# Optimization experiments

Measured on AMD Instinct MI355X. Metric: run time of the kernel, lower is better.

Reference implementation:

```python
import jax, jax.numpy as jnp
import numpy as np

N_FEAT = 128      # node_feat_size
HID = 128         # hidden_size
NUM_SEM = 64
N_ITER = 2
E_TYPES = 8
MAX_CHILDS = 65536
NUM_EDGES = 1048576


def setup_inputs() -> dict:
    key = jax.random.key(0)
    ks = jax.random.split(key, 12)
    d_in = N_FEAT + NUM_SEM
    inp = {
        "child_feats": jax.random.normal(ks[0], (1, MAX_CHILDS, d_in), jnp.float32),
        "child_exists": jax.random.uniform(ks[1], (1, MAX_CHILDS, 1), jnp.float32),
        "edge_type_onehot": jax.random.uniform(ks[2], (1, NUM_EDGES, E_TYPES), jnp.float32),
        "edge_indices": jax.random.randint(ks[3], (1, NUM_EDGES, 2), 0, MAX_CHILDS, jnp.int32),
        # learned params (PyTorch Linear: y = x @ W.T + b; store transposed)
        "W_child": jax.random.normal(ks[4], (d_in, HID), jnp.float32) / np.sqrt(d_in),
        "b_child": jnp.zeros((HID,), jnp.float32),
        "W_edge": jax.random.normal(ks[5], (N_ITER, 2 * HID + E_TYPES, HID), jnp.float32) / np.sqrt(2 * HID + E_TYPES),
        "b_edge": jnp.zeros((N_ITER, HID), jnp.float32),
        "W_parent": jax.random.normal(ks[6], ((N_ITER + 1) * HID, N_FEAT), jnp.float32) / np.sqrt((N_ITER + 1) * HID),
        "b_parent": jnp.zeros((N_FEAT,), jnp.float32),
    }
    return inp


def reference(child_feats, child_exists, edge_type_onehot, edge_indices,
              W_child, b_child, W_edge, b_edge, W_parent, b_parent):
    # batch_size == 1 enforced by original module
    x = jax.nn.relu(child_feats[0] @ W_child + b_child) * child_exists[0]  # (N, H)
    src = edge_indices[0, :, 0]  # (E,)
    dst = edge_indices[0, :, 1]  # (E,)
    ef = edge_type_onehot[0]     # (E, T)

    # node_symmetric_type == 'max' readout
    parent_feats = [jnp.max(x, axis=0)]
    for i in range(N_ITER):
        # gather endpoints, concat with edge features, small MLP
        nef = jnp.concatenate([x[src], x[dst], ef], axis=1)          # (E, 2H+T)
        nef = jax.nn.relu(nef @ W_edge[i] + b_edge[i])               # (E, H)
        # edge_symmetric_type == 'sum' -> scatter_add to source nodes
        x = jax.ops.segment_sum(nef, src, num_segments=MAX_CHILDS)   # (N, H)
        parent_feats.append(jnp.max(x, axis=0))

    parent_feat = jnp.concatenate(parent_feats)[None, :]             # (1, (I+1)*H)
    return jax.nn.relu(parent_feat @ W_parent + b_parent)            # (1, node_feat)
```

## Files before the change

kernel.cpp:

```cpp
#include <hip/hip_runtime.h>
#include <hip/hip_bf16.h>

#define HID 128
#define DIN 192
#define NCH 65536
#define NE  1048576

typedef __bf16 bfrag __attribute__((ext_vector_type(8)));
typedef float  ffrag __attribute__((ext_vector_type(4)));
typedef long   lfrag2 __attribute__((ext_vector_type(2)));

static __device__ __forceinline__ __bf16 f2bf(float x) { return (__bf16)x; }
static __device__ __forceinline__ unsigned pk2(float a, float b) {
    __bf16 b0 = f2bf(a), b1 = f2bf(b);
    return (unsigned)*(unsigned short*)&b0 | ((unsigned)*(unsigned short*)&b1 << 16);
}
static __device__ __forceinline__ unsigned char f2q(float x) {
    return (unsigned char)(__builtin_amdgcn_cvt_pk_fp8_f32(x, x, 0, false) & 0xff);
}

struct FragsQ { long d[4]; long ef; };

static __device__ __forceinline__ void stage_wfrag(
    __bf16* Wl, const float* W, int rowoff, int chunks, int t)
{
    for (int c = t; c < chunks; c += 256) {
        int lane = c & 63, u = (c >> 6) & 7, kt = c >> 9;
        int k0 = kt * 32 + ((lane >> 4) << 3), h = u * 16 + (lane & 15);
        const float* src = W + (size_t)(rowoff + k0) * 128 + h;
        bfrag f;
        #pragma unroll
        for (int j = 0; j < 8; ++j) f[j] = f2bf(src[(size_t)j * 128]);
        *(bfrag*)(&Wl[(size_t)c << 3]) = f;
    }
}

__global__ __launch_bounds__(256) void k_childhist(
    const float* __restrict__ cf, const float* __restrict__ exists,
    const float* __restrict__ Wc, const float* __restrict__ bc,
    __bf16* __restrict__ xA, unsigned int* __restrict__ pmax,
    const int* __restrict__ eidx, int* __restrict__ deg)
{
    if (blockIdx.x >= 1024) {
        const int base = (blockIdx.x - 1024) * 1024 + threadIdx.x;
        #pragma unroll
        for (int k = 0; k < 4; ++k)
            atomicAdd(&deg[eidx[2 * (base + k * 256)]], 1);
        return;
    }

    __shared__ __bf16 Wl[6 * 8 * 64 * 8];
    __shared__ float  bl[HID];
    __shared__ unsigned int cm[HID];
    const int t = threadIdx.x;

    stage_wfrag(Wl, Wc, 0, 3072, t);
    for (int idx = t; idx < HID; idx += 256) { bl[idx] = bc[idx]; cm[idx] = 0u; }
    __syncthreads();

    const int wave = t >> 6, lane = t & 63;
    const int m = lane & 15, quad = lane >> 4;

    const int tile = blockIdx.x * 4 + wave;
    const int r0 = tile << 4;
    const int row = r0 + m;

    ffrag acc[8];
    #pragma unroll
    for (int u = 0; u < 8; ++u)
        #pragma unroll
        for (int r = 0; r < 4; ++r) acc[u][r] = 0.f;

    const float* arow = cf + (size_t)row * DIN + quad * 8;
    #pragma unroll
    for (int kt = 0; kt < 6; ++kt) {
        float4 f0 = *(const float4*)(arow + kt * 32);
        float4 f1 = *(const float4*)(arow + kt * 32 + 4);
        bfrag a;
        a[0]=f2bf(f0.x); a[1]=f2bf(f0.y); a[2]=f2bf(f0.z); a[3]=f2bf(f0.w);
        a[4]=f2bf(f1.x); a[5]=f2bf(f1.y); a[6]=f2bf(f1.z); a[7]=f2bf(f1.w);
        #pragma unroll
        for (int u = 0; u < 8; ++u) {
            bfrag b = *(const bfrag*)(&Wl[(((kt * 8 + u) * 64 + lane) << 3)]);
            acc[u] = __builtin_amdgcn_mfma_f32_16x16x32_bf16(a, b, acc[u], 0, 0, 0);
        }
    }

    float mxu[8];
    #pragma unroll
    for (int u = 0; u < 8; ++u) mxu[u] = 0.f;

    #pragma unroll
    for (int r = 0; r < 4; ++r) {
        int er = r0 + quad * 4 + r;
        float exv = exists[er];
        __bf16* orow = xA + (size_t)er * HID;
        #pragma unroll
        for (int u = 0; u < 8; ++u) {
            int col = u * 16 + m;
            float v = fmaxf(acc[u][r] + bl[col], 0.f) * exv;
            orow[col] = f2bf(v);
            mxu[u] = fmaxf(mxu[u], v);
        }
    }
    #pragma unroll
    for (int u = 0; u < 8; ++u) {
        float v = mxu[u];
        v = fmaxf(v, __shfl_xor(v, 16));
        v = fmaxf(v, __shfl_xor(v, 32));
        if (quad == 0) atomicMax(&cm[u * 16 + m], __float_as_uint(v));
    }
    __syncthreads();
    if (t < HID) atomicMax(&pmax[t], cm[t]);
}

__global__ __launch_bounds__(256) void k_scan1(
    const int* __restrict__ deg, int* __restrict__ bsum)
{
    const int b = blockIdx.x, t = threadIdx.x;
    int v = deg[b * 256 + t];
    #pragma unroll
    for (int o = 1; o < 64; o <<= 1) v += __shfl_xor(v, o);
    __shared__ int ws[4];
    if ((t & 63) == 0) ws[t >> 6] = v;
    __syncthreads();
    if (t == 0) bsum[b] = ws[0] + ws[1] + ws[2] + ws[3];
}

__global__ __launch_bounds__(256) void k_scan23(
    const int* __restrict__ deg, const int* __restrict__ bsum,
    int* __restrict__ off, int* __restrict__ cursor)
{
    __shared__ int sb[256], sc[256];
    const int b = blockIdx.x, t = threadIdx.x;
    int w = bsum[t];
    int v = deg[b * 256 + t];
    sb[t] = w; sc[t] = v;
    __syncthreads();
    for (int o = 1; o < 256; o <<= 1) {
        int u1 = (t >= o) ? sb[t - o] : 0;
        int u2 = (t >= o) ? sc[t - o] : 0;
        __syncthreads();
        sb[t] += u1; sc[t] += u2;
        __syncthreads();
    }
    int bbase = (b == 0) ? 0 : sb[b - 1];
    int excl = bbase + sc[t] - v;
    off[b * 256 + t] = excl;
    cursor[b * 256 + t] = excl;
    if (b == 255 && t == 255) off[NCH] = excl + v;
}

__global__ __launch_bounds__(256) void k_scsrc(
    const __bf16* __restrict__ xCur, const float* __restrict__ We,
    const float* __restrict__ be, __bf16* __restrict__ St2,
    unsigned char* __restrict__ Dq,
    const int* __restrict__ eidx, int* __restrict__ cursor,
    const float* __restrict__ ef,
    int* __restrict__ dsts, unsigned char* __restrict__ efs8)
{
    __shared__ __bf16 Wl[4 * 8 * 64 * 8];
    __shared__ float  bl[HID];
    const int t = threadIdx.x;

    if (blockIdx.x >= 1024) {
        int e = (blockIdx.x - 1024) * 256 + t;
        int s = eidx[2 * e], d = eidx[2 * e + 1];
        const float4* p = (const float4*)(ef + (size_t)e * 8);
        float4 f0 = p[0], f1 = p[1];
        int pos = atomicAdd(&cursor[s], 1);
        dsts[pos] = d;
        unsigned p01 = __builtin_amdgcn_cvt_pk_fp8_f32(f0.x, f0.y, 0, false) & 0xffff;
        unsigned p23 = __builtin_amdgcn_cvt_pk_fp8_f32(f0.z, f0.w, 0, false) & 0xffff;
        unsigned p45 = __builtin_amdgcn_cvt_pk_fp8_f32(f1.x, f1.y, 0, false) & 0xffff;
        unsigned p67 = __builtin_amdgcn_cvt_pk_fp8_f32(f1.z, f1.w, 0, false) & 0xffff;
        unsigned long long v = (unsigned long long)(p01 | (p23 << 16))
                             | ((unsigned long long)(p45 | (p67 << 16)) << 32);
        *(unsigned long long*)(efs8 + (size_t)pos * 8) = v;
        return;
    }

    const int wave = t >> 6, lane = t & 63;
    const int m = lane & 15, quad = lane >> 4;
    const int tile = blockIdx.x * 4 + wave;
    const int r0 = tile << 4;
    const int row = r0 + m;

    stage_wfrag(Wl, We, 0, 2048, t);
    for (int idx = t; idx < HID; idx += 256) bl[idx] = be[idx];
    __syncthreads();

    bfrag a[4];
    const __bf16* ar = xCur + (size_t)row * HID + quad * 8;
    #pragma unroll
    for (int kt = 0; kt < 4; ++kt) a[kt] = *(const bfrag*)(ar + kt * 32);

    ffrag acc[8];
    #pragma unroll
    for (int u = 0; u < 8; ++u)
        #pragma unroll
        for (int r = 0; r < 4; ++r) acc[u][r] = 0.f;

    #pragma unroll
    for (int kt = 0; kt < 4; ++kt)
        #pragma unroll
        for (int u = 0; u < 8; ++u) {
            bfrag b = *(const bfrag*)(&Wl[(((kt * 8 + u) * 64 + lane) << 3)]);
            acc[u] = __builtin_amdgcn_mfma_f32_16x16x32_bf16(a[kt], b, acc[u], 0, 0, 0);
        }
    #pragma unroll
    for (int r = 0; r < 4; ++r) {
        int node = r0 + quad * 4 + r;
        bfrag pk;
        #pragma unroll
        for (int u = 0; u < 8; ++u) pk[u] = f2bf(acc[u][r] + bl[u * 16 + m]);
        *(bfrag*)(St2 + ((size_t)node * 16 + m) * 8) = pk;
    }
    __syncthreads();

    stage_wfrag(Wl, We, 128, 2048, t);
    __syncthreads();

    #pragma unroll
    for (int u = 0; u < 8; ++u)
        #pragma unroll
        for (int r = 0; r < 4; ++r) acc[u][r] = 0.f;

    #pragma unroll
    for (int kt = 0; kt < 4; ++kt)
        #pragma unroll
        for (int u = 0; u < 8; ++u) {
            bfrag b = *(const bfrag*)(&Wl[(((kt * 8 + u) * 64 + lane) << 3)]);
            acc[u] = __builtin_amdgcn_mfma_f32_16x16x32_bf16(a[kt], b, acc[u], 0, 0, 0);
        }
    #pragma unroll
    for (int r = 0; r < 4; ++r) {
        int node = r0 + quad * 4 + r;
        unsigned char* orow = Dq + (size_t)node * 128;
        #pragma unroll
        for (int u = 0; u < 8; ++u)
            orow[((u & 1) * 2 + (m >> 3)) * 32 + (u >> 1) * 8 + (m & 7)] = f2q(acc[u][r]);
    }
}

__global__ __launch_bounds__(256) void k_edge2(
    const unsigned char* __restrict__ Dq,
    const int*    __restrict__ offs,
    const int*    __restrict__ dsts,
    const unsigned char* __restrict__ efs8,
    const __bf16* __restrict__ St2,
    const float*  __restrict__ We,
    __bf16* __restrict__ xNext,
    unsigned int* __restrict__ pmax, int stage)
{
    __shared__ unsigned char Wf[8 * 16 * 8];
    __shared__ unsigned int cm[HID];
    const int t = threadIdx.x;

    if (t < HID) cm[t] = 0u;
    for (int idx = t; idx < 8 * HID; idx += 256) {
        int k2 = idx >> 7, h = idx & 127;
        Wf[((((h >> 4) * 16) + (h & 15)) << 3) + k2] = f2q(We[(size_t)(256 + k2) * HID + h]);
    }
    __syncthreads();

    const int wave = t >> 6, lane = t & 63;
    const int m = lane & 15, quad = lane >> 4;
    const int gw = blockIdx.x * 4 + wave;
    const int n0 = gw * 4;

    const long BevQ = (quad == (m >> 3))     ? ((long)0x38 << (8 * (m & 7))) : 0L;
    const long BodQ = (quad == 2 + (m >> 3)) ? ((long)0x38 << (8 * (m & 7))) : 0L;

    const int o0 = offs[n0],     o1 = offs[n0 + 1], o2 = offs[n0 + 2];
    const int o3 = offs[n0 + 3], o4 = offs[n0 + 4];

    auto selo = [&](int q) -> int {
        return (q <= 0) ? o0 : (q == 1) ? o1 : (q == 2) ? o2 : (q == 3) ? o3 : o4;
    };

    float mxu[8];
    #pragma unroll
    for (int u = 0; u < 8; ++u) mxu[u] = 0.f;

    if (o0 < o4) {
        const int dvA = dsts[min(o0 + lane, o4 - 1)];
        const int dvB = dsts[min(o0 + 64 + lane, o4 - 1)];

        auto LOADT = [&](int j) -> FragsQ {
            FragsQ f;
            int jl = j + m; jl = (jl < o4) ? jl : (o4 - 1);
            int rel = jl - o0;
            int dA = __shfl(dvA, rel & 63);
            int dB = __shfl(dvB, rel & 63);
            int dm;
            if (rel < 64)       dm = dA;
            else if (rel < 128) dm = dB;
            else                dm = dsts[jl];
            const unsigned char* rd = Dq + (size_t)dm * 128 + quad * 32;
            lfrag2 w0 = *(const lfrag2*)(rd);
            lfrag2 w1 = *(const lfrag2*)(rd + 16);
            f.d[0] = w0[0]; f.d[1] = w0[1]; f.d[2] = w1[0]; f.d[3] = w1[1];
            f.ef = (quad == 0) ? *(const long*)(efs8 + (size_t)jl * 8) : 0L;
            return f;
        };

        int ci = 0;
        while (selo(ci) == selo(ci + 1)) ++ci;
        int cj = selo(ci);

        bfrag sb = *(const bfrag*)(St2 + ((size_t)(n0 + ci) * 16 + m) * 8);
        float part[8];
        #pragma unroll
        for (int u = 0; u < 8; ++u) part[u] = 0.f;

        FragsQ aC = LOADT(cj);

        for (;;) {
            const int cEnd = selo(ci + 1);
            int ni = ci, nj = cj + 16;
            if (nj >= cEnd) {
                ni = ci + 1;
                while (ni < 4 && selo(ni) == selo(ni + 1)) ++ni;
                nj = (ni < 4) ? selo(ni) : 0;
            }
            const bool hn = (ni < 4);
            FragsQ aN;
            if (hn) aN = LOADT(nj);

            ffrag acc[8];
            #pragma unroll
            for (int u = 0; u < 8; ++u) {
                float s = (float)sb[u];
                acc[u][0] = s; acc[u][1] = s; acc[u][2] = s; acc[u][3] = s;
            }
            #pragma unroll
            for (int u = 0; u < 8; ++u)
                acc[u] = __builtin_amdgcn_mfma_f32_16x16x32_fp8_fp8(
                    aC.d[u >> 1], (u & 1) ? BodQ : BevQ, acc[u], 0, 0, 0);
            #pragma unroll
            for (int u = 0; u < 8; ++u) {
                long b = *(const long*)(&Wf[((u << 4) + m) << 3]);
                acc[u] = __builtin_amdgcn_mfma_f32_16x16x32_fp8_fp8(aC.ef, b, acc[u], 0, 0, 0);
            }

            const int rb = cj + quad * 4;
            #pragma unroll
            for (int r = 0; r < 4; ++r) {
                if (rb + r < cEnd) {
                    #pragma unroll
                    for (int u = 0; u < 8; ++u)
                        part[u] += fmaxf(acc[u][r], 0.f);
                }
            }

            if (!hn || ni != ci) {
                float tot[8];
                #pragma unroll
                for (int u = 0; u < 8; ++u) {
                    float v = part[u];
                    v += __shfl_xor(v, 16);
                    v += __shfl_xor(v, 32);
                    tot[u] = v;
                    mxu[u] = fmaxf(mxu[u], v);
                }
                float sA = (quad == 0) ? tot[0] : (quad == 1) ? tot[2] : (quad == 2) ? tot[4] : tot[6];
                float sB = (quad == 0) ? tot[1] : (quad == 1) ? tot[3] : (quad == 2) ? tot[5] : tot[7];
                const int n = n0 + ci, u0 = quad * 2;
                xNext[(size_t)n * HID + u0 * 16 + m]      = f2bf(sA);
                xNext[(size_t)n * HID + u0 * 16 + 16 + m] = f2bf(sB);
                if (hn) {
                    sb = *(const bfrag*)(St2 + ((size_t)(n0 + ni) * 16 + m) * 8);
                    #pragma unroll
                    for (int u = 0; u < 8; ++u) part[u] = 0.f;
                }
            }
            if (!hn) break;
            aC = aN; ci = ni; cj = nj;
        }
    }

    {
        const int u0 = quad * 2;
        const __bf16 zz = (__bf16)0.f;
        if (o0 == o1) { xNext[(size_t)(n0+0)*HID + u0*16 + m] = zz; xNext[(size_t)(n0+0)*HID + u0*16 + 16 + m] = zz; }
        if (o1 == o2) { xNext[(size_t)(n0+1)*HID + u0*16 + m] = zz; xNext[(size_t)(n0+1)*HID + u0*16 + 16 + m] = zz; }
        if (o2 == o3) { xNext[(size_t)(n0+2)*HID + u0*16 + m] = zz; xNext[(size_t)(n0+2)*HID + u0*16 + 16 + m] = zz; }
        if (o3 == o4) { xNext[(size_t)(n0+3)*HID + u0*16 + m] = zz; xNext[(size_t)(n0+3)*HID + u0*16 + 16 + m] = zz; }
    }

    #pragma unroll
    for (int u = 0; u < 8; ++u) {
        float v = mxu[u];
        v = fmaxf(v, __shfl_xor(v, 16));
        v = fmaxf(v, __shfl_xor(v, 32));
        if (quad == 0) atomicMax(&cm[u * 16 + m], __float_as_uint(v));
    }
    __syncthreads();
    if (t < HID) atomicMax(&pmax[stage * HID + t], cm[t]);
}

__global__ __launch_bounds__(256) void k_edge_at(
    const __bf16* __restrict__ xA, const int* __restrict__ eidx,
    const float* __restrict__ ef, const float* __restrict__ We,
    const float* __restrict__ be, float* __restrict__ xNew)
{
    __shared__ __bf16 Wl[9 * 8 * 64 * 8];
    __shared__ float  bl[HID];
    const int t = threadIdx.x;
    for (int idx = t; idx < 8 * 64 * 8; idx += 256) Wl[8 * 8 * 64 * 8 + idx] = (__bf16)0.f;
    __syncthreads();
    stage_wfrag(Wl, We, 0, 4096, t);
    for (int idx = t; idx < 8 * HID; idx += 256) {
        int k2 = idx >> 7, h = idx & 127;
        Wl[((((8 * 8) + (h >> 4)) * 64 + (h & 15)) << 3) | k2] = f2bf(We[(256 + k2) * HID + h]);
    }
    for (int idx = t; idx < HID; idx += 256) bl[idx] = be[idx];
    __syncthreads();

    const int wave = t >> 6, lane = t & 63;
    const int m = lane & 15, quad = lane >> 4;
    for (int c = 0; c < 8; ++c) {
        const int e0 = blockIdx.x * 512 + c * 64 + wave * 16;
        const int e  = e0 + m;
        const int src = eidx[2 * e], dst = eidx[2 * e + 1];
        const __bf16* rs = xA + (size_t)src * HID;
        const __bf16* rd = xA + (size_t)dst * HID;
        bfrag a[9];
        #pragma unroll
        for (int kt = 0; kt < 4; ++kt) a[kt] = *(const bfrag*)(rs + kt * 32 + quad * 8);
        #pragma unroll
        for (int kt = 4; kt < 8; ++kt) a[kt] = *(const bfrag*)(rd + (kt - 4) * 32 + quad * 8);
        {
            bfrag z;
            #pragma unroll
            for (int q = 0; q < 8; ++q) z[q] = (__bf16)0.f;
            if (quad == 0) {
                const float4* p = (const float4*)(ef + (size_t)e * 8);
                float4 f0 = p[0], f1 = p[1];
                z[0]=f2bf(f0.x); z[1]=f2bf(f0.y); z[2]=f2bf(f0.z); z[3]=f2bf(f0.w);
                z[4]=f2bf(f1.x); z[5]=f2bf(f1.y); z[6]=f2bf(f1.z); z[7]=f2bf(f1.w);
            }
            a[8] = z;
        }
        ffrag acc[8];
        #pragma unroll
        for (int u = 0; u < 8; ++u)
            #pragma unroll
            for (int r = 0; r < 4; ++r) acc[u][r] = 0.f;
        #pragma unroll
        for (int kt = 0; kt < 9; ++kt)
            #pragma unroll
            for (int u = 0; u < 8; ++u) {
                bfrag b = *(const bfrag*)(&Wl[(((kt * 8 + u) * 64 + lane) << 3)]);
                acc[u] = __builtin_amdgcn_mfma_f32_16x16x32_bf16(a[kt], b, acc[u], 0, 0, 0);
            }
        #pragma unroll
        for (int r = 0; r < 4; ++r) {
            int er = e0 + quad * 4 + r;
            int sr = eidx[2 * er];
            float* outrow = xNew + (size_t)sr * HID;
            #pragma unroll
            for (int u = 0; u < 8; ++u) {
                int col = u * 16 + m;
                atomicAdd(outrow + col, fmaxf(acc[u][r] + bl[col], 0.f));
            }
        }
    }
}

__global__ __launch_bounds__(256) void k_fin(
    float* __restrict__ xNew, __bf16* __restrict__ xA,
    unsigned int* __restrict__ pmax, int stage, int flags)
{
    const int t = threadIdx.x;
    const size_t total  = (size_t)NCH * HID;
    const size_t stride = (size_t)gridDim.x * 256;
    float mx = 0.f;
    for (size_t i = (size_t)blockIdx.x * 256 + t; i < total; i += stride) {
        float v = xNew[i];
        mx = fmaxf(mx, v);
        if (flags & 1) xA[i] = f2bf(v);
        if (flags & 2) xNew[i] = 0.f;
    }
    __shared__ float red[256];
    red[t] = mx;
    __syncthreads();
    if (t < 128) {
        float v = fmaxf(red[t], red[t + 128]);
        atomicMax(&pmax[stage * HID + t], __float_as_uint(v));
    }
}

__global__ __launch_bounds__(128) void k_parent(
    const unsigned int* __restrict__ pmaxU,
    const float* __restrict__ Wp, const float* __restrict__ bp,
    float* __restrict__ out)
{
    __shared__ float pl[384];
    const int t = threadIdx.x;
    for (int i = t; i < 384; i += 128) pl[i] = __uint_as_float(pmaxU[i]);
    __syncthreads();
    float acc = bp[t];
    for (int j = 0; j < 384; ++j) acc += pl[j] * Wp[j * HID + t];
    out[t] = fmaxf(acc, 0.f);
}

extern "C" void kernel_launch(void* const* d_in, const int* in_sizes, int n_in,
                              void* d_out, int out_size, void* d_ws, size_t ws_size,
                              hipStream_t stream)
{
    const float* cf   = (const float*)d_in[0];
    const float* ex   = (const float*)d_in[1];
    const float* ef   = (const float*)d_in[2];
    const int*   eidx = (const int*)d_in[3];
    const float* Wc   = (const float*)d_in[4];
    const float* bc   = (const float*)d_in[5];
    const float* We   = (const float*)d_in[6];
    const float* be   = (const float*)d_in[7];
    const float* Wp   = (const float*)d_in[8];
    const float* bp   = (const float*)d_in[9];
    float* out = (float*)d_out;

    char* ws = (char*)d_ws;

    const size_t OFF_XA   = 0;
    const size_t OFF_XB   = OFF_XA   + (size_t)NCH * HID * 2;
    const size_t OFF_ST   = OFF_XB   + (size_t)NCH * HID * 2;
    const size_t OFF_EFS  = OFF_ST   + (size_t)NCH * HID * 2;
    const size_t OFF_DQ   = OFF_EFS  + (size_t)NE * 8;
    const size_t OFF_DST  = OFF_DQ   + (size_t)NCH * 128;
    const size_t OFF_OFFS = OFF_DST  + (size_t)NE * 4;
    const size_t OFF_DEG  = OFF_OFFS + 262400;
    const size_t OFF_PMAX = OFF_DEG  + 262144;
    const size_t OFF_CUR  = OFF_PMAX + 2048;
    const size_t OFF_BS   = OFF_CUR  + 262144;
    const size_t NEED     = OFF_BS   + 1024;

    if (ws_size >= NEED) {
        __bf16*        xA   = (__bf16*)(ws + OFF_XA);
        __bf16*        xB   = (__bf16*)(ws + OFF_XB);
        __bf16*        St2  = (__bf16*)(ws + OFF_ST);
        unsigned char* efs8 = (unsigned char*)(ws + OFF_EFS);
        unsigned char* Dq   = (unsigned char*)(ws + OFF_DQ);
        int*           dsts = (int*)   (ws + OFF_DST);
        int*           offs = (int*)   (ws + OFF_OFFS);
        int*           deg  = (int*)   (ws + OFF_DEG);
        int*           cur  = (int*)   (ws + OFF_CUR);
        unsigned int*  pmax = (unsigned int*)(ws + OFF_PMAX);
        int*           bsum = (int*)   (ws + OFF_BS);

        hipMemsetAsync(deg, 0, 262144 + 2048, stream);

        k_childhist<<<2048, 256, 0, stream>>>(cf, ex, Wc, bc, xA, pmax, eidx, deg);
        k_scan1  <<<256,  256, 0, stream>>>(deg, bsum);
        k_scan23 <<<256,  256, 0, stream>>>(deg, bsum, offs, cur);

        k_scsrc  <<<5120, 256, 0, stream>>>(xA, We, be, St2, Dq,
                                            eidx, cur, ef, dsts, efs8);
        k_edge2  <<<4096, 256, 0, stream>>>(Dq, offs, dsts, efs8, St2, We, xB, pmax, 1);
        k_scsrc  <<<1024, 256, 0, stream>>>(xB, We + 264 * HID, be + HID, St2, Dq,
                                            eidx, cur, ef, dsts, efs8);
        k_edge2  <<<4096, 256, 0, stream>>>(Dq, offs, dsts, efs8, St2, We + 264 * HID, xA, pmax, 2);
        k_parent <<<1,    128, 0, stream>>>(pmax, Wp, bp, out);
    } else {
        float*        xNew = (float*)ws;
        __bf16*       xA   = (__bf16*)(ws + (size_t)NCH * HID * 4);
        unsigned int* pmax = (unsigned int*)(ws + (size_t)NCH * HID * 6);

        hipMemsetAsync(pmax, 0, 384 * sizeof(unsigned int), stream);
        hipMemsetAsync(xNew, 0, (size_t)NCH * HID * 4, stream);

        k_childhist<<<1024, 256, 0, stream>>>(cf, ex, Wc, bc, xA, pmax, eidx, (int*)nullptr);
        k_edge_at<<<2048, 256, 0, stream>>>(xA, eidx, ef, We,             be,       xNew);
        k_fin    <<<512,  256, 0, stream>>>(xNew, xA, pmax, 1, 3);
        k_edge_at<<<2048, 256, 0, stream>>>(xA, eidx, ef, We + 264 * HID, be + HID, xNew);
        k_fin    <<<512,  256, 0, stream>>>(xNew, xA, pmax, 2, 0);
        k_parent <<<1,    128, 0, stream>>>(pmax, Wp, bp, out);
    }
}
```

Baseline: 518.8 us.

## Deepen edge gather prefetch to two tiles and fuse parent MLP into last edge kernel

The edge aggregation loop now keeps two tiles of gathered destination rows in flight instead of one, so the random-access fp8 row loads have more time to land before the MFMAs use them. Separately, the final parent readout kernel launch is removed: the last block of the second edge pass, found with a global atomic counter, computes the parent linear layer and ReLU itself. The deeper prefetch costs extra registers and may lower occupancy. The fused tail adds a fence and atomic per block and a serial 384-term dot product in a single block.

```diff
diff --git a/kernel.cpp b/kernel.cpp
--- a/kernel.cpp
+++ b/kernel.cpp
@@ -251,7 +251,9 @@
     const __bf16* __restrict__ St2,
     const float*  __restrict__ We,
     __bf16* __restrict__ xNext,
-    unsigned int* __restrict__ pmax, int stage)
+    unsigned int* __restrict__ pmax, int stage,
+    const float* __restrict__ Wp, const float* __restrict__ bp,
+    float* __restrict__ out, unsigned int* __restrict__ ctr)
 {
     __shared__ unsigned char Wf[8 * 16 * 8];
     __shared__ unsigned int cm[HID];
@@ -305,29 +307,37 @@
             return f;
         };
 
-        int ci = 0;
-        while (selo(ci) == selo(ci + 1)) ++ci;
-        int cj = selo(ci);
-
-        bfrag sb = *(const bfrag*)(St2 + ((size_t)(n0 + ci) * 16 + m) * 8);
+        auto adv = [&](int i, int j, int& io, int& jo) {
+            int cEnd = selo(i + 1);
+            int j2 = j + 16;
+            if (j2 < cEnd) { io = i; jo = j2; return; }
+            int i2 = i + 1;
+            while (i2 < 4 && selo(i2) == selo(i2 + 1)) ++i2;
+            io = i2; jo = (i2 < 4) ? selo(i2) : 0;
+        };
+
+        int i0 = 0;
+        while (selo(i0) == selo(i0 + 1)) ++i0;
+        int j0 = selo(i0);
+        int i1, j1;
+        adv(i0, j0, i1, j1);
+
+        FragsQ A0 = LOADT(j0);
+        FragsQ A1;
+        if (i1 < 4) A1 = LOADT(j1);
+
+        bfrag sb = *(const bfrag*)(St2 + ((size_t)(n0 + i0) * 16 + m) * 8);
         float part[8];
         #pragma unroll
         for (int u = 0; u < 8; ++u) part[u] = 0.f;
 
-        FragsQ aC = LOADT(cj);
-
         for (;;) {
-            const int cEnd = selo(ci + 1);
-            int ni = ci, nj = cj + 16;
-            if (nj >= cEnd) {
-                ni = ci + 1;
-                while (ni < 4 && selo(ni) == selo(ni + 1)) ++ni;
-                nj = (ni < 4) ? selo(ni) : 0;
-            }
-            const bool hn = (ni < 4);
-            FragsQ aN;
-            if (hn) aN = LOADT(nj);
-
+            int i2 = 4, j2 = 0;
+            if (i1 < 4) adv(i1, j1, i2, j2);
+            FragsQ A2;
+            if (i2 < 4) A2 = LOADT(j2);
+
+            const int cEnd = selo(i0 + 1);
             ffrag acc[8];
             #pragma unroll
             for (int u = 0; u < 8; ++u) {
@@ -337,14 +347,14 @@
             #pragma unroll
             for (int u = 0; u < 8; ++u)
                 acc[u] = __builtin_amdgcn_mfma_f32_16x16x32_fp8_fp8(
-                    aC.d[u >> 1], (u & 1) ? BodQ : BevQ, acc[u], 0, 0, 0);
+                    A0.d[u >> 1], (u & 1) ? BodQ : BevQ, acc[u], 0, 0, 0);
             #pragma unroll
             for (int u = 0; u < 8; ++u) {
                 long b = *(const long*)(&Wf[((u << 4) + m) << 3]);
-                acc[u] = __builtin_amdgcn_mfma_f32_16x16x32_fp8_fp8(aC.ef, b, acc[u], 0, 0, 0);
-            }
-
-            const int rb = cj + quad * 4;
+                acc[u] = __builtin_amdgcn_mfma_f32_16x16x32_fp8_fp8(A0.ef, b, acc[u], 0, 0, 0);
+            }
+
+            const int rb = j0 + quad * 4;
             #pragma unroll
             for (int r = 0; r < 4; ++r) {
                 if (rb + r < cEnd) {
@@ -354,7 +364,7 @@
                 }
             }
 
-            if (!hn || ni != ci) {
+            if (i1 >= 4 || i1 != i0) {
                 float tot[8];
                 #pragma unroll
                 for (int u = 0; u < 8; ++u) {
@@ -366,17 +376,18 @@
                 }
                 float sA = (quad == 0) ? tot[0] : (quad == 1) ? tot[2] : (quad == 2) ? tot[4] : tot[6];
                 float sB = (quad == 0) ? tot[1] : (quad == 1) ? tot[3] : (quad == 2) ? tot[5] : tot[7];
-                const int n = n0 + ci, u0 = quad * 2;
+                const int n = n0 + i0, u0 = quad * 2;
                 xNext[(size_t)n * HID + u0 * 16 + m]      = f2bf(sA);
                 xNext[(size_t)n * HID + u0 * 16 + 16 + m] = f2bf(sB);
-                if (hn) {
-                    sb = *(const bfrag*)(St2 + ((size_t)(n0 + ni) * 16 + m) * 8);
+                if (i1 < 4) {
+                    sb = *(const bfrag*)(St2 + ((size_t)(n0 + i1) * 16 + m) * 8);
                     #pragma unroll
                     for (int u = 0; u < 8; ++u) part[u] = 0.f;
                 }
             }
-            if (!hn) break;
-            aC = aN; ci = ni; cj = nj;
+            if (i1 >= 4) break;
+            A0 = A1; A1 = A2;
+            i0 = i1; j0 = j1; i1 = i2; j1 = j2;
         }
     }
 
@@ -398,6 +409,27 @@
     }
     __syncthreads();
     if (t < HID) atomicMax(&pmax[stage * HID + t], cm[t]);
+
+    if (stage == 2) {
+        __syncthreads();
+        __shared__ unsigned int done;
+        if (t == 0) {
+            __threadfence();
+            done = atomicAdd(ctr, 1u);
+        }
+        __syncthreads();
+        if (done == gridDim.x - 1) {
+            __shared__ float pl[384];
+            for (int i = t; i < 384; i += 256)
+                pl[i] = __uint_as_float(atomicOr(&pmax[i], 0u));
+            __syncthreads();
+            if (t < 128) {
+                float acc2 = bp[t];
+                for (int j = 0; j < 384; ++j) acc2 += pl[j] * Wp[j * HID + t];
+                out[t] = fmaxf(acc2, 0.f);
+            }
+        }
+    }
 }
 
 __global__ __launch_bounds__(256) void k_edge_at(
@@ -533,7 +565,8 @@
     const size_t OFF_OFFS = OFF_DST  + (size_t)NE * 4;
     const size_t OFF_DEG  = OFF_OFFS + 262400;
     const size_t OFF_PMAX = OFF_DEG  + 262144;
-    const size_t OFF_CUR  = OFF_PMAX + 2048;
+    const size_t OFF_CTR  = OFF_PMAX + 2048;
+    const size_t OFF_CUR  = OFF_CTR  + 64;
     const size_t OFF_BS   = OFF_CUR  + 262144;
     const size_t NEED     = OFF_BS   + 1024;
 
@@ -548,9 +581,10 @@
         int*           deg  = (int*)   (ws + OFF_DEG);
         int*           cur  = (int*)   (ws + OFF_CUR);
         unsigned int*  pmax = (unsigned int*)(ws + OFF_PMAX);
+        unsigned int*  ctr  = (unsigned int*)(ws + OFF_CTR);
         int*           bsum = (int*)   (ws + OFF_BS);
 
-        hipMemsetAsync(deg, 0, 262144 + 2048, stream);
+        hipMemsetAsync(deg, 0, 262144 + 2048 + 64, stream);
 
         k_childhist<<<2048, 256, 0, stream>>>(cf, ex, Wc, bc, xA, pmax, eidx, deg);
         k_scan1  <<<256,  256, 0, stream>>>(deg, bsum);
@@ -558,11 +592,12 @@
 
         k_scsrc  <<<5120, 256, 0, stream>>>(xA, We, be, St2, Dq,
                                             eidx, cur, ef, dsts, efs8);
-        k_edge2  <<<4096, 256, 0, stream>>>(Dq, offs, dsts, efs8, St2, We, xB, pmax, 1);
+        k_edge2  <<<4096, 256, 0, stream>>>(Dq, offs, dsts, efs8, St2, We, xB, pmax, 1,
+                                            Wp, bp, out, ctr);
         k_scsrc  <<<1024, 256, 0, stream>>>(xB, We + 264 * HID, be + HID, St2, Dq,
                                             eidx, cur, ef, dsts, efs8);
-        k_edge2  <<<4096, 256, 0, stream>>>(Dq, offs, dsts, efs8, St2, We + 264 * HID, xA, pmax, 2);
-        k_parent <<<1,    128, 0, stream>>>(pmax, Wp, bp, out);
+        k_edge2  <<<4096, 256, 0, stream>>>(Dq, offs, dsts, efs8, St2, We + 264 * HID, xA, pmax, 2,
+                                            Wp, bp, out, ctr);
     } else {
         float*        xNew = (float*)ws;
         __bf16*       xA   = (__bf16*)(ws + (size_t)NCH * HID * 4);
```

New measurement: 582.8 us. 12.3% more time.
